# Kernel tuning notes

Hardware: AMD Instinct MI355X
Metric: run time of the kernel (lower is better)

The kernel has to match this reference:

```python
import jax, jax.numpy as jnp
import numpy as np

LRELU = 0.2


def _gru(x, Wi, Wh, bi, bh):
    # x: [B,T,D]; Wi: [3H,D]; Wh: [3H,H]; PyTorch GRU equations.
    B, T, D = x.shape
    H = Wh.shape[1]
    xW = jnp.einsum('btd,gd->btg', x, Wi) + bi  # precompute input projections
    def step(h, xw):
        gh = h @ Wh.T + bh
        xr, xz, xn = jnp.split(xw, 3, axis=-1)
        hr, hz, hn = jnp.split(gh, 3, axis=-1)
        r = jax.nn.sigmoid(xr + hr)
        z = jax.nn.sigmoid(xz + hz)
        n = jnp.tanh(xn + r * hn)
        h_new = (1.0 - z) * n + z * h
        return h_new, h_new
    h0 = jnp.zeros((B, H), x.dtype)
    hT, hs = jax.lax.scan(step, h0, jnp.swapaxes(xW, 0, 1))
    return jnp.swapaxes(hs, 0, 1), hT


def _gatv2(x, W, b, a, bias):
    # x: [B,N,F]; W: [2F,E]; lin([v_i||v_j]) == x_i@W1 + x_j@W2 + b (avoids materializing concat)
    F = x.shape[-1]
    W1, W2 = W[:F], W[F:]
    g1 = x @ W1            # [B,N,E]
    g2 = x @ W2 + b        # [B,N,E]
    z = jax.nn.leaky_relu(g1[:, :, None, :] + g2[:, None, :, :], LRELU)  # [B,N,N,E]
    e = jnp.einsum('bije,e->bij', z, a) + bias
    att = jax.nn.softmax(e, axis=2)
    return jax.nn.sigmoid(jnp.einsum('bij,bjf->bif', att, x))


def setup_inputs() -> dict:
    B, W, K, H, KS = 16, 256, 64, 150, 7
    key = jax.random.key(0)
    ks = jax.random.split(key, 32)
    def rn(i, sh, scale):
        return jax.random.normal(ks[i], sh, jnp.float32) * scale
    inp = {}
    inp['x'] = jax.random.normal(ks[0], (B, W, K), jnp.float32)
    inp['conv_w'] = rn(1, (K, K, KS), 1.0 / np.sqrt(K * KS))
    inp['conv_b'] = rn(2, (K,), 0.02)
    inp['fW'] = rn(3, (2 * W, 2 * W), 1.0 / np.sqrt(2 * W))
    inp['fb'] = rn(4, (2 * W,), 0.02)
    inp['fa'] = rn(5, (2 * W,), 1.0 / np.sqrt(2 * W))
    inp['fbias'] = rn(6, (K, K), 0.02)
    inp['tW'] = rn(7, (2 * K, 2 * K), 1.0 / np.sqrt(2 * K))
    inp['tb'] = rn(8, (2 * K,), 0.02)
    inp['ta'] = rn(9, (2 * K,), 1.0 / np.sqrt(2 * K))
    inp['tbias'] = rn(10, (W, W), 0.02)
    inp['gWi'] = rn(11, (3 * H, 3 * K), 1.0 / np.sqrt(H))
    inp['gWh'] = rn(12, (3 * H, H), 1.0 / np.sqrt(H))
    inp['gbi'] = rn(13, (3 * H,), 0.02)
    inp['gbh'] = rn(14, (3 * H,), 0.02)
    inp['f0w'] = rn(15, (H, H), 1.0 / np.sqrt(H))
    inp['f0b'] = rn(16, (H,), 0.02)
    inp['f1w'] = rn(17, (H, K), 1.0 / np.sqrt(H))
    inp['f1b'] = rn(18, (K,), 0.02)
    inp['rWi'] = rn(19, (3 * H, H), 1.0 / np.sqrt(H))
    inp['rWh'] = rn(20, (3 * H, H), 1.0 / np.sqrt(H))
    inp['rbi'] = rn(21, (3 * H,), 0.02)
    inp['rbh'] = rn(22, (3 * H,), 0.02)
    inp['rfw'] = rn(23, (H, K), 1.0 / np.sqrt(H))
    inp['rfb'] = rn(24, (K,), 0.02)
    return inp


def reference(x, conv_w, conv_b, fW, fb, fa, fbias, tW, tb, ta, tbias,
              gWi, gWh, gbi, gbh, f0w, f0b, f1w, f1b,
              rWi, rWh, rbi, rbh, rfw, rfb):
    B, Wsz, K = x.shape
    pad = (conv_w.shape[2] - 1) // 2
    # ConvLayer: permute -> constant pad -> conv1d -> relu -> permute back
    x_ncw = jnp.swapaxes(x, 1, 2)  # [B,K,W]
    x_pad = jnp.pad(x_ncw, ((0, 0), (0, 0), (pad, pad)))
    xc = jax.lax.conv_general_dilated(x_pad, conv_w, (1,), 'VALID',
                                      dimension_numbers=('NCW', 'OIW', 'NCW'))
    xc = jax.nn.relu(xc + conv_b[None, :, None])
    xc = jnp.swapaxes(xc, 1, 2)  # [B,W,K]
    # Feature GAT over nodes (K), temporal GAT over time (W)
    h_feat = jnp.swapaxes(_gatv2(jnp.swapaxes(xc, 1, 2), fW, fb, fa, fbias), 1, 2)  # [B,W,K]
    h_temp = _gatv2(xc, tW, tb, ta, tbias)  # [B,W,K]
    h_cat = jnp.concatenate([xc, h_feat, h_temp], axis=2)  # [B,W,3K]
    _, h_end = _gru(h_cat, gWi, gWh, gbi, gbh)  # [B,H]
    # Forecasting MLP (n_layers=1 -> two Linear layers)
    predictions = jax.nn.relu(h_end @ f0w + f0b) @ f1w + f1b  # [B,K]
    # Reconstruction: repeat_interleave over dim 1 then view(B, W, -1)
    H = h_end.shape[1]
    h_rep = jnp.repeat(h_end, Wsz, axis=1).reshape(B, Wsz, H)
    dec_out, _ = _gru(h_rep, rWi, rWh, rbi, rbh)  # [B,W,H]
    recons = dec_out @ rfw + rfb  # [B,W,K]
    return predictions, recons
```

## Files before the change

kernel.cpp:

```cpp
#include <hip/hip_runtime.h>
#include <hip/hip_fp16.h>

typedef _Float16 h2f __attribute__((ext_vector_type(2)));

__device__ __forceinline__ float dot2f(unsigned a, unsigned b, float c) {
#if __has_builtin(__builtin_amdgcn_fdot2)
  return __builtin_amdgcn_fdot2(__builtin_bit_cast(h2f, a),
                                __builtin_bit_cast(h2f, b), c, false);
#else
  h2f x = __builtin_bit_cast(h2f, a);
  h2f y = __builtin_bit_cast(h2f, b);
  return c + (float)x[0] * (float)y[0] + (float)x[1] * (float)y[1];
#endif
}

__device__ __forceinline__ float sigf(float x) { return 1.0f / (1.0f + __expf(-x)); }
__device__ __forceinline__ float tanhfast(float x) {
  float e = __expf(-2.0f * fabsf(x));
  float r = (1.0f - e) / (1.0f + e);
  return (x < 0.0f) ? -r : r;
}
__device__ __forceinline__ float lrelu(float x) { return x > 0.0f ? x : 0.2f * x; }

__global__ void k_prep(const float* __restrict__ conv_w, const float* __restrict__ gWi,
                       const float* __restrict__ gWh, const float* __restrict__ rWh,
                       const float* __restrict__ rWi,
                       float* __restrict__ cwT, float* __restrict__ gWiT,
                       unsigned* __restrict__ gWhP, unsigned* __restrict__ rWhP,
                       float* __restrict__ pref) {
  const int N0 = 64 * 64 * 7;
  const int N1 = 192 * 450;
  const int N2 = 76 * 450;
  const int N3 = 76 * 450;
  const int N4 = 450;
  int total = N0 + N1 + N2 + N3 + N4;
  for (int idx = blockIdx.x * blockDim.x + threadIdx.x; idx < total;
       idx += gridDim.x * blockDim.x) {
    if (idx < N0) {
      int k = idx & 63; int is = idx >> 6; int i = is / 7; int s = is - i * 7;
      cwT[idx] = conv_w[(k * 64 + i) * 7 + s];
    } else if (idx < N0 + N1) {
      int j = idx - N0; int g = j % 450; int d = j / 450;
      gWiT[j] = gWi[g * 192 + d];
    } else if (idx < N0 + N1 + N2) {
      int j = idx - (N0 + N1); int g = j % 450; int jj = j / 450;
      int j0 = 2 * jj, j1 = 2 * jj + 1;
      float a = (j0 < 150) ? gWh[g * 150 + j0] : 0.f;
      float b = (j1 < 150) ? gWh[g * 150 + j1] : 0.f;
      __half2 h = __floats2half2_rn(a, b);
      gWhP[j] = *reinterpret_cast<unsigned*>(&h);
    } else if (idx < N0 + N1 + N2 + N3) {
      int j = idx - (N0 + N1 + N2); int g = j % 450; int jj = j / 450;
      int j0 = 2 * jj, j1 = 2 * jj + 1;
      float a = (j0 < 150) ? rWh[g * 150 + j0] : 0.f;
      float b = (j1 < 150) ? rWh[g * 150 + j1] : 0.f;
      __half2 h = __floats2half2_rn(a, b);
      rWhP[j] = *reinterpret_cast<unsigned*>(&h);
    } else {
      int g = idx - (N0 + N1 + N2 + N3);
      float run = 0.f;
      pref[g] = 0.f;
      for (int j = 0; j < 150; ++j) { run += rWi[g * 150 + j]; pref[(j + 1) * 450 + g] = run; }
    }
  }
}

__global__ __launch_bounds__(256) void k_conv(const float* __restrict__ x,
                                              const float* __restrict__ cwT,
                                              const float* __restrict__ conv_b,
                                              float* __restrict__ xc) {
  __shared__ float xs[22 * 64];
  int b = blockIdx.y, t0 = blockIdx.x * 16, tid = threadIdx.x;
  for (int l = tid; l < 22 * 64; l += 256) {
    int r = l >> 6, i = l & 63;
    int t = t0 - 3 + r;
    xs[l] = (t >= 0 && t < 256) ? x[(b * 256 + t) * 64 + i] : 0.f;
  }
  __syncthreads();
  int k = tid & 63, tg = tid >> 6;
  float bias = conv_b[k];
  float acc[4] = {bias, bias, bias, bias};
  for (int i = 0; i < 64; ++i) {
#pragma unroll
    for (int s = 0; s < 7; ++s) {
      float wv = cwT[(i * 7 + s) * 64 + k];
#pragma unroll
      for (int q = 0; q < 4; ++q)
        acc[q] += xs[(tg * 4 + q + s) * 64 + i] * wv;
    }
  }
#pragma unroll
  for (int q = 0; q < 4; ++q)
    xc[(b * 256 + t0 + tg * 4 + q) * 64 + k] = fmaxf(acc[q], 0.f);
}

__global__ __launch_bounds__(512) void k_featg(const float* __restrict__ xc,
                                               const float* __restrict__ fW,
                                               const float* __restrict__ fb,
                                               float* __restrict__ g1f,
                                               float* __restrict__ g2fT) {
  __shared__ float xsL[256 * 8];
  int b = blockIdx.y, i0 = blockIdx.x * 8, e = threadIdx.x;
  for (int l = e; l < 2048; l += 512) {
    int t = l >> 3, ii = l & 7;
    xsL[l] = xc[(b * 256 + t) * 64 + i0 + ii];
  }
  __syncthreads();
  float a1[8] = {}, a2[8] = {};
  for (int t = 0; t < 256; ++t) {
    float w1 = fW[t * 512 + e];
    float w2 = fW[(256 + t) * 512 + e];
#pragma unroll
    for (int ii = 0; ii < 8; ++ii) {
      float s = xsL[t * 8 + ii];
      a1[ii] += s * w1; a2[ii] += s * w2;
    }
  }
  float fbe = fb[e];
#pragma unroll
  for (int ii = 0; ii < 8; ++ii)
    g1f[(b * 64 + i0 + ii) * 512 + e] = a1[ii];
  float4 v0 = make_float4(a2[0] + fbe, a2[1] + fbe, a2[2] + fbe, a2[3] + fbe);
  float4 v1 = make_float4(a2[4] + fbe, a2[5] + fbe, a2[6] + fbe, a2[7] + fbe);
  float4* p = reinterpret_cast<float4*>(&g2fT[(b * 512 + e) * 64 + i0]);
  p[0] = v0; p[1] = v1;
}

__global__ __launch_bounds__(256) void k_feata(const float* __restrict__ xc,
                                               const float* __restrict__ g1f,
                                               const float* __restrict__ g2fT,
                                               const float* __restrict__ fa,
                                               const float* __restrict__ fbias,
                                               float* __restrict__ h_feat) {
  __shared__ float g1L[512], faL[512], part[4 * 64], attL[64];
  int b = blockIdx.y, i = blockIdx.x, tid = threadIdx.x;
  for (int l = tid; l < 512; l += 256) {
    g1L[l] = g1f[(b * 64 + i) * 512 + l];
    faL[l] = fa[l];
  }
  __syncthreads();
  int q = tid >> 6, j = tid & 63;
  float acc = 0.f;
  for (int e = q * 128; e < q * 128 + 128; ++e) {
    float z = g1L[e] + g2fT[(b * 512 + e) * 64 + j];
    acc += faL[e] * lrelu(z);
  }
  part[q * 64 + j] = acc;
  __syncthreads();
  if (tid < 64) {
    float ev = part[tid] + part[64 + tid] + part[128 + tid] + part[192 + tid] +
               fbias[i * 64 + tid];
    float m = ev;
#pragma unroll
    for (int off = 32; off > 0; off >>= 1) m = fmaxf(m, __shfl_xor(m, off));
    float p = __expf(ev - m);
    float s = p;
#pragma unroll
    for (int off = 32; off > 0; off >>= 1) s += __shfl_xor(s, off);
    attL[tid] = p / s;
  }
  __syncthreads();
  float o = 0.f;
  for (int jj = 0; jj < 64; ++jj)
    o += attL[jj] * xc[(b * 256 + tid) * 64 + jj];
  h_feat[(b * 256 + tid) * 64 + i] = sigf(o);
}

__global__ __launch_bounds__(256) void k_tempg(const float* __restrict__ xc,
                                               const float* __restrict__ tW,
                                               const float* __restrict__ tb,
                                               float* __restrict__ g1t,
                                               float* __restrict__ g2tT) {
  __shared__ float xsL[16 * 64];
  int b = blockIdx.y, t0 = blockIdx.x * 16, tid = threadIdx.x;
  int e = tid & 127, th = tid >> 7;
  for (int l = tid; l < 1024; l += 256)
    xsL[l] = xc[(b * 256 + t0) * 64 + l];
  __syncthreads();
  float a1[8] = {}, a2[8] = {};
  for (int k = 0; k < 64; ++k) {
    float w1 = tW[k * 128 + e];
    float w2 = tW[(64 + k) * 128 + e];
#pragma unroll
    for (int tt = 0; tt < 8; ++tt) {
      float s = xsL[(th * 8 + tt) * 64 + k];
      a1[tt] += s * w1; a2[tt] += s * w2;
    }
  }
  float tbe = tb[e];
#pragma unroll
  for (int tt = 0; tt < 8; ++tt)
    g1t[(b * 256 + t0 + th * 8 + tt) * 128 + e] = a1[tt];
  float4 v0 = make_float4(a2[0] + tbe, a2[1] + tbe, a2[2] + tbe, a2[3] + tbe);
  float4 v1 = make_float4(a2[4] + tbe, a2[5] + tbe, a2[6] + tbe, a2[7] + tbe);
  float4* p = reinterpret_cast<float4*>(&g2tT[(b * 128 + e) * 256 + t0 + th * 8]);
  p[0] = v0; p[1] = v1;
}

__global__ __launch_bounds__(256) void k_tempa(const float* __restrict__ xc,
                                               const float* __restrict__ g1t,
                                               const float* __restrict__ g2tT,
                                               const float* __restrict__ ta,
                                               const float* __restrict__ tbias,
                                               float* __restrict__ h_temp) {
  __shared__ float g1L[4 * 128], taL[128], eL[4 * 256];
  int b = blockIdx.y, i0 = blockIdx.x * 4, tid = threadIdx.x;
  for (int l = tid; l < 512; l += 256)
    g1L[l] = g1t[(b * 256 + i0) * 128 + l];
  if (tid < 128) taL[tid] = ta[tid];
  __syncthreads();
  float acc[4] = {};
  for (int e = 0; e < 128; ++e) {
    float g2 = g2tT[(b * 128 + e) * 256 + tid];
    float tae = taL[e];
#pragma unroll
    for (int ii = 0; ii < 4; ++ii)
      acc[ii] += tae * lrelu(g1L[ii * 128 + e] + g2);
  }
#pragma unroll
  for (int ii = 0; ii < 4; ++ii)
    eL[ii * 256 + tid] = acc[ii] + tbias[(i0 + ii) * 256 + tid];
  __syncthreads();
  int wv = tid >> 6, ln = tid & 63;
  {
    float v0 = eL[wv * 256 + ln], v1 = eL[wv * 256 + 64 + ln];
    float v2 = eL[wv * 256 + 128 + ln], v3 = eL[wv * 256 + 192 + ln];
    float m = fmaxf(fmaxf(v0, v1), fmaxf(v2, v3));
#pragma unroll
    for (int off = 32; off > 0; off >>= 1) m = fmaxf(m, __shfl_xor(m, off));
    float p0 = __expf(v0 - m), p1 = __expf(v1 - m);
    float p2 = __expf(v2 - m), p3 = __expf(v3 - m);
    float s = p0 + p1 + p2 + p3;
#pragma unroll
    for (int off = 32; off > 0; off >>= 1) s += __shfl_xor(s, off);
    float rs = 1.f / s;
    eL[wv * 256 + ln] = p0 * rs; eL[wv * 256 + 64 + ln] = p1 * rs;
    eL[wv * 256 + 128 + ln] = p2 * rs; eL[wv * 256 + 192 + ln] = p3 * rs;
  }
  __syncthreads();
  int ii = tid >> 6, k = tid & 63;
  float o = 0.f;
  for (int j = 0; j < 256; ++j)
    o += eL[ii * 256 + j] * xc[(b * 256 + j) * 64 + k];
  h_temp[(b * 256 + i0 + ii) * 64 + k] = sigf(o);
}

__global__ __launch_bounds__(256) void k_xw(const float* __restrict__ xc,
                                            const float* __restrict__ h_feat,
                                            const float* __restrict__ h_temp,
                                            const float* __restrict__ gWiT,
                                            const float* __restrict__ gbi,
                                            float* __restrict__ xW) {
  __shared__ float hc[16 * 192];
  int b = blockIdx.z, t0 = blockIdx.y * 16, g0 = blockIdx.x * 128;
  int tid = threadIdx.x;
  for (int l = tid; l < 16 * 192; l += 256) {
    int tt = l / 192, d = l - tt * 192;
    int row = (b * 256 + t0 + tt) * 64;
    float v;
    if (d < 64) v = xc[row + d];
    else if (d < 128) v = h_feat[row + d - 64];
    else v = h_temp[row + d - 128];
    hc[l] = v;
  }
  __syncthreads();
  int gl = tid & 127, th = tid >> 7;
  int g = g0 + gl;
  if (g < 450) {
    float acc[8] = {};
    for (int d = 0; d < 192; ++d) {
      float w = gWiT[d * 450 + g];
#pragma unroll
      for (int tt = 0; tt < 8; ++tt)
        acc[tt] += hc[(th * 8 + tt) * 192 + d] * w;
    }
    float bi = gbi[g];
#pragma unroll
    for (int tt = 0; tt < 8; ++tt)
      xW[(b * 256 + t0 + th * 8 + tt) * 450 + g] = acc[tt] + bi;
  }
}

__global__ __launch_bounds__(512, 2) void k_gru(const float* __restrict__ xwAll,
                                                const unsigned* __restrict__ WhP,
                                                const float* __restrict__ bh,
                                                const float* __restrict__ pref,
                                                const float* __restrict__ rbi,
                                                const float* __restrict__ h_end_in,
                                                float* __restrict__ h_end,
                                                float* __restrict__ dec_out,
                                                int mode) {
  __shared__ __align__(16) unsigned hPair[80];
  __shared__ float hL32[152], rL[152], zL[152], heL[152];
  int b = blockIdx.x, tid = threadIdx.x;
  if (tid < 80) hPair[tid] = 0u;
  if (tid < 152) hL32[tid] = 0.f;
  unsigned w[76];
  float bhv = 0.f;
  if (tid < 450) {
#pragma unroll
    for (int jj = 0; jj < 76; ++jj) w[jj] = WhP[jj * 450 + tid];
    bhv = bh[tid];
  }
  const float* xwrow = xwAll + (size_t)(b * 256) * 450;
  float tot = 0.f, bi = 0.f;
  if (mode == 1) {
    if (tid < 152) heL[tid] = (tid < 150) ? h_end_in[b * 150 + tid] : 0.f;
    if (tid < 450) { tot = pref[150 * 450 + tid]; bi = rbi[tid]; }
  }
  __syncthreads();

  auto ldraw = [&](int t) -> float {
    if (mode == 0) return xwrow[t * 450 + tid];
    int base = 150 * t; int a = base >> 8;
    int c = 256 * (a + 1) - base; if (c > 150) c = 150;
    return pref[c * 450 + tid];
  };

  const uint4* hp4 = reinterpret_cast<const uint4*>(hPair);
  float r0 = 0.f, r1 = 0.f;
  if (tid < 450) { r0 = ldraw(0); r1 = ldraw(1); }

  for (int t = 0; t < 256; ++t) {
    float rf = 0.f;
    if (tid < 450 && t + 2 < 256) rf = ldraw(t + 2);
    float a0 = bhv, a1 = 0.f, a2 = 0.f, a3 = 0.f;
    if (tid < 450) {
#pragma unroll
      for (int q = 0; q < 19; ++q) {
        uint4 hv = hp4[q];
        a0 = dot2f(hv.x, w[4 * q + 0], a0);
        a1 = dot2f(hv.y, w[4 * q + 1], a1);
        a2 = dot2f(hv.z, w[4 * q + 2], a2);
        a3 = dot2f(hv.w, w[4 * q + 3], a3);
      }
    }
    float acc = (a0 + a1) + (a2 + a3);
    float xwv = 0.f;
    if (tid < 450) {
      if (mode == 0) {
        xwv = r0;
      } else {
        int base = 150 * t; int a = base >> 8;
        xwv = bi + heL[a] * r0 + heL[a + 1] * (tot - r0);
      }
    }
    if (tid < 150) rL[tid] = sigf(xwv + acc);
    else if (tid < 300) zL[tid - 150] = sigf(xwv + acc);
    __syncthreads();
    if (tid >= 300 && tid < 450) {
      int i2 = tid - 300;
      float n = tanhfast(xwv + rL[i2] * acc);
      float z = zL[i2];
      float hn = (1.f - z) * n + z * hL32[i2];
      hL32[i2] = hn;
      reinterpret_cast<__half*>(hPair)[i2] = __float2half(hn);
      if (mode == 1) dec_out[((size_t)(b * 256) + t) * 150 + i2] = hn;
    }
    __syncthreads();
    r0 = r1; r1 = rf;
  }
  if (mode == 0 && tid < 150) h_end[b * 150 + tid] = hL32[tid];
}

__global__ __launch_bounds__(192) void k_pred(const float* __restrict__ h_end,
                                              const float* __restrict__ f0w,
                                              const float* __restrict__ f0b,
                                              const float* __restrict__ f1w,
                                              const float* __restrict__ f1b,
                                              float* __restrict__ out) {
  __shared__ float heL[152], t1L[152];
  int b = blockIdx.x, tid = threadIdx.x;
  if (tid < 152) heL[tid] = (tid < 150) ? h_end[b * 150 + tid] : 0.f;
  __syncthreads();
  if (tid < 150) {
    float a = f0b[tid];
    for (int i = 0; i < 150; ++i) a += heL[i] * f0w[i * 150 + tid];
    t1L[tid] = fmaxf(a, 0.f);
  }
  if (tid >= 150 && tid < 152) t1L[tid] = 0.f;
  __syncthreads();
  if (tid < 64) {
    float a = f1b[tid];
    for (int j = 0; j < 150; ++j) a += t1L[j] * f1w[j * 64 + tid];
    out[b * 64 + tid] = a;
  }
}

__global__ __launch_bounds__(256) void k_recon(const float* __restrict__ dec_out,
                                               const float* __restrict__ rfw,
                                               const float* __restrict__ rfb,
                                               float* __restrict__ out) {
  int row = blockIdx.x * 4 + (threadIdx.x >> 6);
  int k = threadIdx.x & 63;
  const float* d = dec_out + (size_t)row * 150;
  float a = rfb[k];
  for (int j = 0; j < 150; ++j) a += d[j] * rfw[j * 64 + k];
  out[1024 + (size_t)row * 64 + k] = a;
}

extern "C" void kernel_launch(void* const* d_in, const int* in_sizes, int n_in,
                              void* d_out, int out_size, void* d_ws, size_t ws_size,
                              hipStream_t stream) {
  (void)in_sizes; (void)n_in; (void)out_size; (void)ws_size;
  const float* x      = (const float*)d_in[0];
  const float* conv_w = (const float*)d_in[1];
  const float* conv_b = (const float*)d_in[2];
  const float* fW     = (const float*)d_in[3];
  const float* fb     = (const float*)d_in[4];
  const float* fa     = (const float*)d_in[5];
  const float* fbias  = (const float*)d_in[6];
  const float* tW     = (const float*)d_in[7];
  const float* tb     = (const float*)d_in[8];
  const float* ta     = (const float*)d_in[9];
  const float* tbias  = (const float*)d_in[10];
  const float* gWi    = (const float*)d_in[11];
  const float* gWh    = (const float*)d_in[12];
  const float* gbi    = (const float*)d_in[13];
  const float* gbh    = (const float*)d_in[14];
  const float* f0w    = (const float*)d_in[15];
  const float* f0b    = (const float*)d_in[16];
  const float* f1w    = (const float*)d_in[17];
  const float* f1b    = (const float*)d_in[18];
  const float* rWi    = (const float*)d_in[19];
  const float* rWh    = (const float*)d_in[20];
  const float* rbi    = (const float*)d_in[21];
  const float* rbh    = (const float*)d_in[22];
  const float* rfw    = (const float*)d_in[23];
  const float* rfb    = (const float*)d_in[24];
  float* out = (float*)d_out;
  float* ws  = (float*)d_ws;

  float* XC   = ws;
  float* HF   = XC + 262144;
  float* HT   = HF + 262144;
  float* GBUF = HT + 262144;
  float* G1F  = GBUF;
  float* G2FT = GBUF + 524288;
  float* G1T  = GBUF + 1048576;
  float* G2TT = GBUF + 1572864;
  float* XW   = GBUF;
  float* HEND = GBUF + 2097152;
  float* DEC  = HEND + 2400;
  float* CWT  = DEC + 614400;
  float* GWIT = CWT + 28672;
  unsigned* GWHP = (unsigned*)(GWIT + 86400);
  unsigned* RWHP = GWHP + 34200;
  float* PREF = (float*)(RWHP + 34200);

  k_prep<<<512, 256, 0, stream>>>(conv_w, gWi, gWh, rWh, rWi, CWT, GWIT, GWHP, RWHP, PREF);
  k_conv<<<dim3(16, 16), 256, 0, stream>>>(x, CWT, conv_b, XC);
  k_featg<<<dim3(8, 16), 512, 0, stream>>>(XC, fW, fb, G1F, G2FT);
  k_tempg<<<dim3(16, 16), 256, 0, stream>>>(XC, tW, tb, G1T, G2TT);
  k_feata<<<dim3(64, 16), 256, 0, stream>>>(XC, G1F, G2FT, fa, fbias, HF);
  k_tempa<<<dim3(64, 16), 256, 0, stream>>>(XC, G1T, G2TT, ta, tbias, HT);
  k_xw<<<dim3(4, 16, 16), 256, 0, stream>>>(XC, HF, HT, GWIT, gbi, XW);
  k_gru<<<16, 512, 0, stream>>>(XW, GWHP, gbh, nullptr, nullptr, nullptr, HEND, nullptr, 0);
  k_pred<<<16, 192, 0, stream>>>(HEND, f0w, f0b, f1w, f1b, out);
  k_gru<<<16, 512, 0, stream>>>(nullptr, RWHP, rbh, PREF, rbi, HEND, nullptr, DEC, 1);
  k_recon<<<1024, 256, 0, stream>>>(DEC, rfw, rfb, out);
}
```

Before: 718.5 us.

## Restructure GRU recurrence: 4 lanes per hidden unit, shuffle reduce, one barrier

The GRU kernel now assigns each hidden unit to four adjacent lanes. Each lane holds the r, z and n weight slices as packed half2 uint4 registers, and the partial dot products are combined with xor shuffles. Because every thread then computes all three gates for its unit, the shared r/z staging and the second __syncthreads per timestep go away, and a double-buffered fp16 hidden vector removes the read/write hazard. Weight prepacking changes to match the new layout and the block grows to 640 threads. The sequential critical path per step should shrink, at the cost of three times the gate math and more threads.

Measured after the change: 754.0 us. +4.9%, slower.

```diff
diff --git a/kernel.cpp b/kernel.cpp
--- a/kernel.cpp
+++ b/kernel.cpp
@@ -30,8 +30,8 @@
                        float* __restrict__ pref) {
   const int N0 = 64 * 64 * 7;
   const int N1 = 192 * 450;
-  const int N2 = 76 * 450;
-  const int N3 = 76 * 450;
+  const int N2 = 36000;
+  const int N3 = 36000;
   const int N4 = 450;
   int total = N0 + N1 + N2 + N3 + N4;
   for (int idx = blockIdx.x * blockDim.x + threadIdx.x; idx < total;
@@ -42,20 +42,22 @@
     } else if (idx < N0 + N1) {
       int j = idx - N0; int g = j % 450; int d = j / 450;
       gWiT[j] = gWi[g * 192 + d];
-    } else if (idx < N0 + N1 + N2) {
-      int j = idx - (N0 + N1); int g = j % 450; int jj = j / 450;
-      int j0 = 2 * jj, j1 = 2 * jj + 1;
-      float a = (j0 < 150) ? gWh[g * 150 + j0] : 0.f;
-      float b = (j1 < 150) ? gWh[g * 150 + j1] : 0.f;
+    } else if (idx < N0 + N1 + N2 + N3) {
+      int u = idx - (N0 + N1);
+      const float* W = gWh;
+      unsigned* dst = gWhP;
+      if (u >= N2) { u -= N2; W = rWh; dst = rWhP; }
+      int c = u & 3; int q = u >> 2;
+      int i = q / 600; int t6 = q - i * 600;
+      int i2 = t6 >> 2, qt = t6 & 3;
+      int gg = i / 5, li = i - gg * 5;
+      int jj = qt * 20 + li * 4 + c;
+      int e0 = 2 * jj, e1 = 2 * jj + 1;
+      int row = i2 + gg * 150;
+      float a = (e0 < 150) ? W[row * 150 + e0] : 0.f;
+      float b = (e1 < 150) ? W[row * 150 + e1] : 0.f;
       __half2 h = __floats2half2_rn(a, b);
-      gWhP[j] = *reinterpret_cast<unsigned*>(&h);
-    } else if (idx < N0 + N1 + N2 + N3) {
-      int j = idx - (N0 + N1 + N2); int g = j % 450; int jj = j / 450;
-      int j0 = 2 * jj, j1 = 2 * jj + 1;
-      float a = (j0 < 150) ? rWh[g * 150 + j0] : 0.f;
-      float b = (j1 < 150) ? rWh[g * 150 + j1] : 0.f;
-      __half2 h = __floats2half2_rn(a, b);
-      rWhP[j] = *reinterpret_cast<unsigned*>(&h);
+      dst[u] = *reinterpret_cast<unsigned*>(&h);
     } else {
       int g = idx - (N0 + N1 + N2 + N3);
       float run = 0.f;
@@ -281,8 +283,8 @@
   }
 }
 
-__global__ __launch_bounds__(512, 2) void k_gru(const float* __restrict__ xwAll,
-                                                const unsigned* __restrict__ WhP,
+__global__ __launch_bounds__(640, 3) void k_gru(const float* __restrict__ xwAll,
+                                                const uint4* __restrict__ WhP4,
                                                 const float* __restrict__ bh,
                                                 const float* __restrict__ pref,
                                                 const float* __restrict__ rbi,
@@ -290,77 +292,94 @@
                                                 float* __restrict__ h_end,
                                                 float* __restrict__ dec_out,
                                                 int mode) {
-  __shared__ __align__(16) unsigned hPair[80];
-  __shared__ float hL32[152], rL[152], zL[152], heL[152];
+  __shared__ __align__(16) unsigned hPair[2][80];
+  __shared__ float heL[152];
   int b = blockIdx.x, tid = threadIdx.x;
-  if (tid < 80) hPair[tid] = 0u;
-  if (tid < 152) hL32[tid] = 0.f;
-  unsigned w[76];
-  float bhv = 0.f;
-  if (tid < 450) {
-#pragma unroll
-    for (int jj = 0; jj < 76; ++jj) w[jj] = WhP[jj * 450 + tid];
-    bhv = bh[tid];
-  }
-  const float* xwrow = xwAll + (size_t)(b * 256) * 450;
-  float tot = 0.f, bi = 0.f;
+  bool act = tid < 600;
+  int t6 = act ? tid : 0;
+  int i2 = t6 >> 2, qt = t6 & 3;
+  for (int l = tid; l < 160; l += 640) (&hPair[0][0])[l] = 0u;
+
+  uint4 wv[15];
+#pragma unroll
+  for (int i = 0; i < 15; ++i) wv[i] = WhP4[i * 600 + t6];
+  float bh3[3], bi3[3] = {0.f, 0.f, 0.f}, tot3[3] = {0.f, 0.f, 0.f};
+#pragma unroll
+  for (int gg = 0; gg < 3; ++gg) bh3[gg] = bh[i2 + gg * 150];
   if (mode == 1) {
     if (tid < 152) heL[tid] = (tid < 150) ? h_end_in[b * 150 + tid] : 0.f;
-    if (tid < 450) { tot = pref[150 * 450 + tid]; bi = rbi[tid]; }
-  }
-  __syncthreads();
-
-  auto ldraw = [&](int t) -> float {
-    if (mode == 0) return xwrow[t * 450 + tid];
-    int base = 150 * t; int a = base >> 8;
-    int c = 256 * (a + 1) - base; if (c > 150) c = 150;
-    return pref[c * 450 + tid];
+#pragma unroll
+    for (int gg = 0; gg < 3; ++gg) {
+      bi3[gg] = rbi[i2 + gg * 150];
+      tot3[gg] = pref[150 * 450 + i2 + gg * 150];
+    }
+  }
+  const float* xwrow = xwAll ? (xwAll + (size_t)b * 256 * 450) : nullptr;
+
+  auto ld3 = [&](int t, float* dst) {
+    if (mode == 0) {
+      const float* p = xwrow + t * 450 + i2;
+#pragma unroll
+      for (int gg = 0; gg < 3; ++gg) dst[gg] = p[gg * 150];
+    } else {
+      int base = 150 * t; int a = base >> 8;
+      int c = 256 * (a + 1) - base; if (c > 150) c = 150;
+      const float* p = pref + c * 450 + i2;
+#pragma unroll
+      for (int gg = 0; gg < 3; ++gg) dst[gg] = p[gg * 150];
+    }
   };
 
-  const uint4* hp4 = reinterpret_cast<const uint4*>(hPair);
-  float r0 = 0.f, r1 = 0.f;
-  if (tid < 450) { r0 = ldraw(0); r1 = ldraw(1); }
-
+  float p0[3], p1[3] = {0.f, 0.f, 0.f};
+  ld3(0, p0);
+  __syncthreads();
+
+  float hprev = 0.f;
+  int buf = 0;
+  const uint4* hp4 = reinterpret_cast<const uint4*>(&hPair[0][0]);
   for (int t = 0; t < 256; ++t) {
-    float rf = 0.f;
-    if (tid < 450 && t + 2 < 256) rf = ldraw(t + 2);
-    float a0 = bhv, a1 = 0.f, a2 = 0.f, a3 = 0.f;
-    if (tid < 450) {
-#pragma unroll
-      for (int q = 0; q < 19; ++q) {
-        uint4 hv = hp4[q];
-        a0 = dot2f(hv.x, w[4 * q + 0], a0);
-        a1 = dot2f(hv.y, w[4 * q + 1], a1);
-        a2 = dot2f(hv.z, w[4 * q + 2], a2);
-        a3 = dot2f(hv.w, w[4 * q + 3], a3);
-      }
-    }
-    float acc = (a0 + a1) + (a2 + a3);
-    float xwv = 0.f;
-    if (tid < 450) {
-      if (mode == 0) {
-        xwv = r0;
-      } else {
-        int base = 150 * t; int a = base >> 8;
-        xwv = bi + heL[a] * r0 + heL[a + 1] * (tot - r0);
-      }
-    }
-    if (tid < 150) rL[tid] = sigf(xwv + acc);
-    else if (tid < 300) zL[tid - 150] = sigf(xwv + acc);
+    if (t + 1 < 256) ld3(t + 1, p1);
+    float ar = 0.f, ar2 = 0.f, az = 0.f, az2 = 0.f, an = 0.f, an2 = 0.f;
+#pragma unroll
+    for (int i = 0; i < 5; ++i) {
+      uint4 hv = hp4[buf * 20 + qt * 5 + i];
+      ar  = dot2f(hv.x, wv[i].x, ar);        ar2 = dot2f(hv.y, wv[i].y, ar2);
+      ar  = dot2f(hv.z, wv[i].z, ar);        ar2 = dot2f(hv.w, wv[i].w, ar2);
+      az  = dot2f(hv.x, wv[5 + i].x, az);    az2 = dot2f(hv.y, wv[5 + i].y, az2);
+      az  = dot2f(hv.z, wv[5 + i].z, az);    az2 = dot2f(hv.w, wv[5 + i].w, az2);
+      an  = dot2f(hv.x, wv[10 + i].x, an);   an2 = dot2f(hv.y, wv[10 + i].y, an2);
+      an  = dot2f(hv.z, wv[10 + i].z, an);   an2 = dot2f(hv.w, wv[10 + i].w, an2);
+    }
+    ar += ar2; az += az2; an += an2;
+    ar += __shfl_xor(ar, 1); ar += __shfl_xor(ar, 2);
+    az += __shfl_xor(az, 1); az += __shfl_xor(az, 2);
+    an += __shfl_xor(an, 1); an += __shfl_xor(an, 2);
+    ar += bh3[0]; az += bh3[1]; an += bh3[2];
+
+    float xr, xz, xn;
+    if (mode == 0) {
+      xr = p0[0]; xz = p0[1]; xn = p0[2];
+    } else {
+      int base = 150 * t; int a = base >> 8;
+      float hA = heL[a], hB = heL[a + 1];
+      xr = bi3[0] + hA * p0[0] + hB * (tot3[0] - p0[0]);
+      xz = bi3[1] + hA * p0[1] + hB * (tot3[1] - p0[1]);
+      xn = bi3[2] + hA * p0[2] + hB * (tot3[2] - p0[2]);
+    }
+    float r = sigf(xr + ar);
+    float z = sigf(xz + az);
+    float n = tanhfast(xn + r * an);
+    float hn = (1.f - z) * n + z * hprev;
+    hprev = hn;
+    if (act && qt == 0) {
+      reinterpret_cast<__half*>(&hPair[buf ^ 1][0])[i2] = __float2half(hn);
+      if (mode == 1) dec_out[((size_t)(b * 256) + t) * 150 + i2] = hn;
+    }
+    p0[0] = p1[0]; p0[1] = p1[1]; p0[2] = p1[2];
+    buf ^= 1;
     __syncthreads();
-    if (tid >= 300 && tid < 450) {
-      int i2 = tid - 300;
-      float n = tanhfast(xwv + rL[i2] * acc);
-      float z = zL[i2];
-      float hn = (1.f - z) * n + z * hL32[i2];
-      hL32[i2] = hn;
-      reinterpret_cast<__half*>(hPair)[i2] = __float2half(hn);
-      if (mode == 1) dec_out[((size_t)(b * 256) + t) * 150 + i2] = hn;
-    }
-    __syncthreads();
-    r0 = r1; r1 = rf;
-  }
-  if (mode == 0 && tid < 150) h_end[b * 150 + tid] = hL32[tid];
+  }
+  if (mode == 0 && act && qt == 0) h_end[b * 150 + i2] = hprev;
 }
 
 __global__ __launch_bounds__(192) void k_pred(const float* __restrict__ h_end,
@@ -445,8 +464,8 @@
   float* CWT  = DEC + 614400;
   float* GWIT = CWT + 28672;
   unsigned* GWHP = (unsigned*)(GWIT + 86400);
-  unsigned* RWHP = GWHP + 34200;
-  float* PREF = (float*)(RWHP + 34200);
+  unsigned* RWHP = GWHP + 36000;
+  float* PREF = (float*)(RWHP + 36000);
 
   k_prep<<<512, 256, 0, stream>>>(conv_w, gWi, gWh, rWh, rWi, CWT, GWIT, GWHP, RWHP, PREF);
   k_conv<<<dim3(16, 16), 256, 0, stream>>>(x, CWT, conv_b, XC);
@@ -455,8 +474,8 @@
   k_feata<<<dim3(64, 16), 256, 0, stream>>>(XC, G1F, G2FT, fa, fbias, HF);
   k_tempa<<<dim3(64, 16), 256, 0, stream>>>(XC, G1T, G2TT, ta, tbias, HT);
   k_xw<<<dim3(4, 16, 16), 256, 0, stream>>>(XC, HF, HT, GWIT, gbi, XW);
-  k_gru<<<16, 512, 0, stream>>>(XW, GWHP, gbh, nullptr, nullptr, nullptr, HEND, nullptr, 0);
+  k_gru<<<16, 640, 0, stream>>>(XW, (const uint4*)GWHP, gbh, nullptr, nullptr, nullptr, HEND, nullptr, 0);
   k_pred<<<16, 192, 0, stream>>>(HEND, f0w, f0b, f1w, f1b, out);
-  k_gru<<<16, 512, 0, stream>>>(nullptr, RWHP, rbh, PREF, rbi, HEND, nullptr, DEC, 1);
+  k_gru<<<16, 640, 0, stream>>>(nullptr, (const uint4*)RWHP, rbh, PREF, rbi, HEND, nullptr, DEC, 1);
   k_recon<<<1024, 256, 0, stream>>>(DEC, rfw, rfb, out);
 }
```
